# Optimization experiments

Measured on AMD Instinct MI355X. Metric: run time of the kernel, lower is better.

## Reference

```python
import jax, jax.numpy as jnp
import numpy as np

N, E, C, EC, L = 50000, 600000, 128, 16, 4
LN_EPS = 1e-5


def setup_inputs() -> dict:
    key = jax.random.key(0)
    ks = jax.random.split(key, 10)
    return {
        "x": jax.random.normal(ks[0], (N, C), jnp.float32),
        "edge_attr": jax.random.normal(ks[1], (E, EC), jnp.float32),
        "We": jax.random.normal(ks[2], (EC, C), jnp.float32) / np.sqrt(EC).astype(np.float32),
        "be": jnp.zeros((C,), jnp.float32),
        "W1": jax.random.normal(ks[3], (L, C, C), jnp.float32) / np.sqrt(C).astype(np.float32),
        "b1": jnp.zeros((L, C), jnp.float32),
        "W2": jax.random.normal(ks[4], (L, C, C), jnp.float32) / np.sqrt(C).astype(np.float32),
        "b2": jnp.zeros((L, C), jnp.float32),
        "gamma": jnp.ones((L, C), jnp.float32),
        "beta": jnp.zeros((L, C), jnp.float32),
        "edge_index": jax.random.randint(ks[5], (2, E), 0, N, dtype=jnp.int32),
    }


def reference(x, edge_attr, We, be, W1, b1, W2, b2, gamma, beta, edge_index):
    src = edge_index[0]  # x_j (message source)
    dst = edge_index[1]  # aggregation target
    # lin_edge: Linear + SiLU, shared across layers
    ea = jax.nn.silu(edge_attr @ We + be)  # [E, C]
    n = x.shape[0]
    for l in range(L):
        # GINEConv message: ReLU(x_j + edge_attr), scatter-sum to target nodes
        msg = jax.nn.relu(x[src] + ea)                       # [E, C]
        agg = jax.ops.segment_sum(msg, dst, num_segments=n)  # [N, C]
        h = x + agg  # (1 + eps) * x + agg, eps = 0
        # GINEConv nn: Linear -> SiLU -> Linear
        h = jax.nn.silu(h @ W1[l] + b1[l]) @ W2[l] + b2[l]
        # residual + LayerNorm
        y = x + h
        mu = y.mean(-1, keepdims=True)
        var = y.var(-1, keepdims=True)
        x = (y - mu) * jax.lax.rsqrt(var + LN_EPS) * gamma[l] + beta[l]
    return x
```

## Files before the change

kernel.cpp:

```cpp
#include <hip/hip_runtime.h>

#define NN 50000
#define EE 600000
#define CC 128
#define ECC 16
#define LL 4
#define LN_EPS 1e-5f
#define MTILE 80
#define PADC 136
#define YSTR 132

typedef float f32x4 __attribute__((ext_vector_type(4)));
typedef short bf16x8 __attribute__((ext_vector_type(8)));

static __device__ __forceinline__ float bf2f(unsigned short u) {
  union { unsigned int i; float f; } v; v.i = ((unsigned int)u) << 16; return v.f;
}
static __device__ __forceinline__ unsigned short f2bf(float f) {
  union { float f; unsigned int i; } v; v.f = f;
  unsigned int b = v.i + 0x7FFFu + ((v.i >> 16) & 1u);
  return (unsigned short)(b >> 16);
}
static __device__ __forceinline__ float silu_f(float v) {
  return v / (1.f + __expf(-v));
}


__global__ void count_kernel(const int* __restrict__ dst, int* __restrict__ counts, int E) {
  int e = blockIdx.x * blockDim.x + threadIdx.x;
  if (e < E) atomicAdd(&counts[dst[e]], 1);
}

__global__ __launch_bounds__(1024) void scan1_kernel(const int* __restrict__ counts,
                                                     int* __restrict__ bsum, int n) {
  __shared__ int wsum[16];
  const int tid = threadIdx.x, lane = tid & 63, wv = tid >> 6;
  const int i = blockIdx.x * 1024 + tid;
  int s = (i < n) ? counts[i] : 0;
  #pragma unroll
  for (int off = 1; off < 64; off <<= 1) s += __shfl_xor(s, off);
  if (lane == 0) wsum[wv] = s;
  __syncthreads();
  if (tid == 0) {
    int t = 0;
    #pragma unroll
    for (int j = 0; j < 16; ++j) t += wsum[j];
    bsum[blockIdx.x] = t;
  }
}

__global__ void scan2_kernel(const int* __restrict__ bsum, int* __restrict__ boff, int nb) {
  const int lane = threadIdx.x;
  int v = (lane < nb) ? bsum[lane] : 0;
  int incl = v;
  #pragma unroll
  for (int off = 1; off < 64; off <<= 1) {
    int t = __shfl_up(incl, off);
    if (lane >= off) incl += t;
  }
  if (lane < nb) boff[lane] = incl - v;
}

__global__ __launch_bounds__(1024) void scan3_kernel(const int* __restrict__ counts,
                                                     const int* __restrict__ boff,
                                                     int* __restrict__ rowptr, int n) {
  __shared__ int wsum[16];
  const int tid = threadIdx.x, lane = tid & 63, wv = tid >> 6;
  const int i = blockIdx.x * 1024 + tid;
  const int v = (i < n) ? counts[i] : 0;
  int incl = v;
  #pragma unroll
  for (int off = 1; off < 64; off <<= 1) {
    int t = __shfl_up(incl, off);
    if (lane >= off) incl += t;
  }
  if (lane == 63) wsum[wv] = incl;
  __syncthreads();
  if (wv == 0) {
    int vv = (lane < 16) ? wsum[lane] : 0;
    int vi = vv;
    #pragma unroll
    for (int off = 1; off < 16; off <<= 1) {
      int t = __shfl_up(vi, off);
      if (lane >= off) vi += t;
    }
    if (lane < 16) wsum[lane] = vi - vv;
  }
  __syncthreads();
  if (i < n) rowptr[i + 1] = boff[blockIdx.x] + wsum[wv] + incl;
  if (i == 0) rowptr[0] = 0;
}

__global__ void fill_kernel(const int* __restrict__ src, const int* __restrict__ dst,
                            const int* __restrict__ rowptr, int* __restrict__ cursor,
                            int* __restrict__ eidx, int* __restrict__ esrc, int E) {
  int e = blockIdx.x * blockDim.x + threadIdx.x;
  if (e < E) {
    const int d = dst[e];
    const int pos = rowptr[d] + atomicAdd(&cursor[d], 1);
    eidx[pos] = e;
    esrc[pos] = src[e];
  }
}


__global__ void webconv_kernel(const float* __restrict__ We, unsigned short* __restrict__ webf) {
  const int t = blockIdx.x * blockDim.x + threadIdx.x;
  if (t >= 8 * 64 * 8) return;
  const int j = t & 7, l = (t >> 3) & 63, cg = t >> 9;
  const int k = (l >> 4) * 8 + j, c = cg * 16 + (l & 15);
  webf[t] = (k < 16) ? f2bf(We[k * CC + c]) : (unsigned short)0;
}


__global__ __launch_bounds__(256) void ea_kernel(const float* __restrict__ edge_attr,
                                                 const unsigned short* __restrict__ webf,
                                                 const float* __restrict__ be,
                                                 const int* __restrict__ eidx,
                                                 unsigned short* __restrict__ ea) {
  __shared__ float er[64][20];
  __shared__ unsigned short eaT[64 * 132];
  const int tid = threadIdx.x;
  const int lane = tid & 63, wv = tid >> 6;

  bf16x8 bw[8];
  #pragma unroll
  for (int cg = 0; cg < 8; ++cg)
    bw[cg] = *(const bf16x8*)(webf + cg * 512 + lane * 8);
  float bev[8];
  #pragma unroll
  for (int cg = 0; cg < 8; ++cg) bev[cg] = be[cg * 16 + (lane & 15)];

  const int base = blockIdx.x * 64;
  {
    const int r = tid >> 2, q = tid & 3;
    const int e = eidx[base + r];
    *(float4*)(&er[r][q * 4]) = *(const float4*)(edge_attr + (size_t)e * ECC + q * 4);
  }
  __syncthreads();

  const int arow = wv * 16 + (lane & 15);
  const int ko = lane >> 4;
  union { unsigned short u[8]; bf16x8 v; } afu;
  if (ko < 2) {
    #pragma unroll
    for (int j = 0; j < 8; ++j) afu.u[j] = f2bf(er[arow][ko * 8 + j]);
  } else {
    #pragma unroll
    for (int j = 0; j < 8; ++j) afu.u[j] = 0;
  }

  f32x4 acc[8];
  #pragma unroll
  for (int cg = 0; cg < 8; ++cg) {
    acc[cg] = (f32x4)0.f;
    acc[cg] = __builtin_amdgcn_mfma_f32_16x16x32_bf16(afu.v, bw[cg], acc[cg], 0, 0, 0);
  }

  const int rl0 = wv * 16 + ko * 4;
  const int cb = lane & 15;
  #pragma unroll
  for (int cg = 0; cg < 8; ++cg)
    #pragma unroll
    for (int r = 0; r < 4; ++r) {
      const float v = acc[cg][r] + bev[cg];
      eaT[(rl0 + r) * 132 + cg * 16 + cb] = f2bf(silu_f(v));
    }
  __syncthreads();

  uint4* eg = (uint4*)(ea + (size_t)base * CC);
  #pragma unroll
  for (int k = 0; k < 4; ++k) {
    const int u = tid + k * 256;
    const int row = u >> 4, ch = u & 15;
    eg[u] = *(const uint4*)(&eaT[row * 132 + ch * 8]);
  }
}


__global__ __launch_bounds__(128) void wconv_kernel(const float* __restrict__ W1,
                                                    const float* __restrict__ W2,
                                                    unsigned short* __restrict__ wt) {
  const int b = blockIdx.x;
  const int c = b & (CC - 1);
  const int mat = (b >> 7) & 1;
  const int l = b >> 8;
  const float* W = (mat ? W2 : W1) + (size_t)l * CC * CC;
  unsigned short* o = wt + ((size_t)l * 2 + mat) * CC * CC + (size_t)c * CC;
  const int k = threadIdx.x;
  o[k] = f2bf(W[(size_t)k * CC + c]);
}


__global__ __launch_bounds__(256) void agg4_kernel(const float* __restrict__ x_in,
                                                   unsigned short* __restrict__ h_out,
                                                   const unsigned short* __restrict__ ea,
                                                   const int* __restrict__ rowptr,
                                                   const int* __restrict__ esrc) {
  const int tid = threadIdx.x;
  const int lane = tid & 63;
  const int half = lane >> 5;
  const int l32 = lane & 31;
  const int c0 = l32 * 4;
  const int wv = tid >> 6;
  const int n = blockIdx.x * 4 + wv;

  const int p0 = rowptr[n], p1 = rowptr[n + 1];
  float a0 = 0.f, a1 = 0.f, a2 = 0.f, a3 = 0.f;

  int p = p0 + half;
  for (; p + 2 < p1; p += 4) {
    const int s0 = esrc[p], s1 = esrc[p + 2];
    const float4 x0 = *(const float4*)(x_in + (size_t)s0 * CC + c0);
    const float4 x1 = *(const float4*)(x_in + (size_t)s1 * CC + c0);
    const uint2 e0 = *(const uint2*)(ea + (size_t)p * CC + c0);
    const uint2 e1 = *(const uint2*)(ea + (size_t)(p + 2) * CC + c0);
    a0 += fmaxf(x0.x + bf2f((unsigned short)e0.x), 0.f)
        + fmaxf(x1.x + bf2f((unsigned short)e1.x), 0.f);
    a1 += fmaxf(x0.y + bf2f((unsigned short)(e0.x >> 16)), 0.f)
        + fmaxf(x1.y + bf2f((unsigned short)(e1.x >> 16)), 0.f);
    a2 += fmaxf(x0.z + bf2f((unsigned short)e0.y), 0.f)
        + fmaxf(x1.z + bf2f((unsigned short)e1.y), 0.f);
    a3 += fmaxf(x0.w + bf2f((unsigned short)(e0.y >> 16)), 0.f)
        + fmaxf(x1.w + bf2f((unsigned short)(e1.y >> 16)), 0.f);
  }
  if (p < p1) {
    const int s0 = esrc[p];
    const float4 x0 = *(const float4*)(x_in + (size_t)s0 * CC + c0);
    const uint2 e0 = *(const uint2*)(ea + (size_t)p * CC + c0);
    a0 += fmaxf(x0.x + bf2f((unsigned short)e0.x), 0.f);
    a1 += fmaxf(x0.y + bf2f((unsigned short)(e0.x >> 16)), 0.f);
    a2 += fmaxf(x0.z + bf2f((unsigned short)e0.y), 0.f);
    a3 += fmaxf(x0.w + bf2f((unsigned short)(e0.y >> 16)), 0.f);
  }

  a0 += __shfl_xor(a0, 32);
  a1 += __shfl_xor(a1, 32);
  a2 += __shfl_xor(a2, 32);
  a3 += __shfl_xor(a3, 32);

  if (half == 0) {
    const float4 xs = *(const float4*)(x_in + (size_t)n * CC + c0);
    uint2 pk;
    pk.x = (unsigned int)f2bf(xs.x + a0) | ((unsigned int)f2bf(xs.y + a1) << 16);
    pk.y = (unsigned int)f2bf(xs.z + a2) | ((unsigned int)f2bf(xs.w + a3) << 16);
    *(uint2*)(h_out + (size_t)n * CC + c0) = pk;
  }
}


__global__ __launch_bounds__(256) void agg_fb_kernel(const float* __restrict__ x_in,
                                                     unsigned short* __restrict__ h_out,
                                                     const float* __restrict__ edge_attr,
                                                     const float* __restrict__ We,
                                                     const float* __restrict__ be,
                                                     const int* __restrict__ rowptr,
                                                     const int* __restrict__ eidx,
                                                     const int* __restrict__ esrc) {
  const int tid = threadIdx.x;
  const int c = tid & (CC - 1);
  const int g = tid >> 7;
  const int n = blockIdx.x * 2 + g;

  float wec[ECC];
  #pragma unroll
  for (int k = 0; k < ECC; ++k) wec[k] = We[k * CC + c];
  const float bev = be[c];

  const int p0 = rowptr[n], p1 = rowptr[n + 1];
  float acc = 0.f;
  for (int p = p0; p < p1; ++p) {
    const int e0 = eidx[p];
    const int s0 = esrc[p];
    const float4* ar0 = (const float4*)(edge_attr + (size_t)e0 * ECC);
    const float4 a0 = ar0[0], a1 = ar0[1], a2 = ar0[2], a3 = ar0[3];
    float v0 = bev
      + a0.x*wec[0]  + a0.y*wec[1]  + a0.z*wec[2]  + a0.w*wec[3]
      + a1.x*wec[4]  + a1.y*wec[5]  + a1.z*wec[6]  + a1.w*wec[7]
      + a2.x*wec[8]  + a2.y*wec[9]  + a2.z*wec[10] + a2.w*wec[11]
      + a3.x*wec[12] + a3.y*wec[13] + a3.z*wec[14] + a3.w*wec[15];
    acc += fmaxf(x_in[(size_t)s0 * CC + c] + silu_f(v0), 0.f);
  }
  h_out[(size_t)n * CC + c] = f2bf(x_in[(size_t)n * CC + c] + acc);
}


__global__ __launch_bounds__(256) void mlp_kernel(const float* __restrict__ x_in,
                                                  const unsigned short* __restrict__ hbuf,
                                                  const unsigned short* __restrict__ wt1,
                                                  const unsigned short* __restrict__ wt2,
                                                  const float* __restrict__ b1,
                                                  const float* __restrict__ b2,
                                                  const float* __restrict__ gamma,
                                                  const float* __restrict__ beta,
                                                  float* __restrict__ x_out) {
  __shared__ __align__(16) char smem[MTILE * PADC * 2 * 2];
  unsigned short* hA = (unsigned short*)smem;
  unsigned short* tA = (unsigned short*)(smem + MTILE * PADC * 2);
  float* yS = (float*)smem;
  __shared__ float red[MTILE][4][2];

  const int tid = threadIdx.x;
  const int lane = tid & 63;
  const int wv = tid >> 6;
  const int node0 = blockIdx.x * MTILE;
  const int colq = lane & 15;
  const int krow = lane >> 4;
  const int colb = wv * 32;

  for (int idx = tid; idx < MTILE * 16; idx += 256) {
    const int row = idx >> 4, ch = idx & 15;
    *(uint4*)(&hA[row * PADC + ch * 8]) =
        *(const uint4*)(hbuf + (size_t)(node0 + row) * CC + ch * 8);
  }
  __syncthreads();

  bf16x8 bw[2][4];
  #pragma unroll
  for (int n2 = 0; n2 < 2; ++n2)
    #pragma unroll
    for (int kk = 0; kk < 4; ++kk)
      bw[n2][kk] = *(const bf16x8*)(wt1 + (size_t)(colb + n2 * 16 + colq) * CC + kk * 32 + krow * 8);

  f32x4 acc[5][2];
  #pragma unroll
  for (int m = 0; m < 5; ++m) { acc[m][0] = (f32x4)0.f; acc[m][1] = (f32x4)0.f; }

  #pragma unroll
  for (int m = 0; m < 5; ++m)
    #pragma unroll
    for (int kk = 0; kk < 4; ++kk) {
      const bf16x8 a = *(const bf16x8*)(&hA[(m * 16 + colq) * PADC + kk * 32 + krow * 8]);
      acc[m][0] = __builtin_amdgcn_mfma_f32_16x16x32_bf16(a, bw[0][kk], acc[m][0], 0, 0, 0);
      acc[m][1] = __builtin_amdgcn_mfma_f32_16x16x32_bf16(a, bw[1][kk], acc[m][1], 0, 0, 0);
    }

  const float b1v0 = b1[colb + colq], b1v1 = b1[colb + 16 + colq];
  #pragma unroll
  for (int m = 0; m < 5; ++m)
    #pragma unroll
    for (int r = 0; r < 4; ++r) {
      const int row = m * 16 + krow * 4 + r;
      tA[row * PADC + colb + colq]      = f2bf(silu_f(acc[m][0][r] + b1v0));
      tA[row * PADC + colb + 16 + colq] = f2bf(silu_f(acc[m][1][r] + b1v1));
    }
  __syncthreads();

  #pragma unroll
  for (int n2 = 0; n2 < 2; ++n2)
    #pragma unroll
    for (int kk = 0; kk < 4; ++kk)
      bw[n2][kk] = *(const bf16x8*)(wt2 + (size_t)(colb + n2 * 16 + colq) * CC + kk * 32 + krow * 8);

  f32x4 acc2[5][2];
  #pragma unroll
  for (int m = 0; m < 5; ++m) { acc2[m][0] = (f32x4)0.f; acc2[m][1] = (f32x4)0.f; }

  #pragma unroll
  for (int m = 0; m < 5; ++m)
    #pragma unroll
    for (int kk = 0; kk < 4; ++kk) {
      const bf16x8 a = *(const bf16x8*)(&tA[(m * 16 + colq) * PADC + kk * 32 + krow * 8]);
      acc2[m][0] = __builtin_amdgcn_mfma_f32_16x16x32_bf16(a, bw[0][kk], acc2[m][0], 0, 0, 0);
      acc2[m][1] = __builtin_amdgcn_mfma_f32_16x16x32_bf16(a, bw[1][kk], acc2[m][1], 0, 0, 0);
    }

  const float b2v0 = b2[colb + colq], b2v1 = b2[colb + 16 + colq];
  float yv[5][2][4];
  #pragma unroll
  for (int m = 0; m < 5; ++m)
    #pragma unroll
    for (int r = 0; r < 4; ++r) {
      const int row = m * 16 + krow * 4 + r;
      yv[m][0][r] = acc2[m][0][r] + b2v0 + x_in[(size_t)(node0 + row) * CC + colb + colq];
      yv[m][1][r] = acc2[m][1][r] + b2v1 + x_in[(size_t)(node0 + row) * CC + colb + 16 + colq];
    }

  #pragma unroll
  for (int m = 0; m < 5; ++m)
    #pragma unroll
    for (int r = 0; r < 4; ++r) {
      float s = yv[m][0][r] + yv[m][1][r];
      float s2 = yv[m][0][r] * yv[m][0][r] + yv[m][1][r] * yv[m][1][r];
      #pragma unroll
      for (int off = 1; off < 16; off <<= 1) {
        s  += __shfl_xor(s, off);
        s2 += __shfl_xor(s2, off);
      }
      if (colq == 0) {
        const int row = m * 16 + krow * 4 + r;
        red[row][wv][0] = s;
        red[row][wv][1] = s2;
      }
    }
  __syncthreads();

  const float gm0 = gamma[colb + colq], gm1 = gamma[colb + 16 + colq];
  const float bt0 = beta[colb + colq],  bt1 = beta[colb + 16 + colq];
  #pragma unroll
  for (int m = 0; m < 5; ++m)
    #pragma unroll
    for (int r = 0; r < 4; ++r) {
      const int row = m * 16 + krow * 4 + r;
      const float s  = red[row][0][0] + red[row][1][0] + red[row][2][0] + red[row][3][0];
      const float s2 = red[row][0][1] + red[row][1][1] + red[row][2][1] + red[row][3][1];
      const float mean = s * (1.f / 128.f);
      const float var = s2 * (1.f / 128.f) - mean * mean;
      const float rstd = rsqrtf(var + LN_EPS);
      yS[row * YSTR + colb + colq]      = (yv[m][0][r] - mean) * rstd * gm0 + bt0;
      yS[row * YSTR + colb + 16 + colq] = (yv[m][1][r] - mean) * rstd * gm1 + bt1;
    }
  __syncthreads();

  float* og = x_out + (size_t)node0 * CC;
  #pragma unroll
  for (int k = 0; k < 10; ++k) {
    const int u = tid + k * 256;
    const int row = u >> 5, q = u & 31;
    *(float4*)(og + u * 4) = *(const float4*)(&yS[row * YSTR + q * 4]);
  }
}


extern "C" void kernel_launch(void* const* d_in, const int* in_sizes, int n_in,
                              void* d_out, int out_size, void* d_ws, size_t ws_size,
                              hipStream_t stream) {
  const float* x         = (const float*)d_in[0];
  const float* edge_attr = (const float*)d_in[1];
  const float* We        = (const float*)d_in[2];
  const float* be        = (const float*)d_in[3];
  const float* W1        = (const float*)d_in[4];
  const float* b1        = (const float*)d_in[5];
  const float* W2        = (const float*)d_in[6];
  const float* b2        = (const float*)d_in[7];
  const float* gamma     = (const float*)d_in[8];
  const float* beta      = (const float*)d_in[9];
  const int*   ei        = (const int*)d_in[10];
  const int*   src       = ei;
  const int*   dst       = ei + EE;
  float* out = (float*)d_out;

  char* ws = (char*)d_ws;
  float*          xbuf   = (float*)(ws + 0);
  unsigned short* hbuf   = (unsigned short*)(ws + 25600000);
  unsigned short* wt     = (unsigned short*)(ws + 38400000);
  int*            counts = (int*)(ws + 38662400);
  int*            rowptr = (int*)(ws + 38862592);
  int*            cursor = (int*)(ws + 39062784);
  int*            eidx   = (int*)(ws + 39262976);
  int*            esrc   = (int*)(ws + 41663232);
  unsigned short* ea     = (unsigned short*)(ws + 44063232);
  unsigned short* webf   = (unsigned short*)(ws + 39062784);
  int*            bsum   = (int*)(ws + 39262976);
  int*            boff   = (int*)(ws + 39262976 + 256);
  const bool use_ea = (ws_size >= 197663232ull);
  const int NB = (NN + 1023) / 1024;

  hipMemsetAsync(counts, 0, (size_t)NN * 4, stream);
  hipMemsetAsync(cursor, 0, (size_t)NN * 4, stream);
  count_kernel<<<(EE + 255) / 256, 256, 0, stream>>>(dst, counts, EE);
  scan1_kernel<<<NB, 1024, 0, stream>>>(counts, bsum, NN);
  scan2_kernel<<<1, 64, 0, stream>>>(bsum, boff, NB);
  scan3_kernel<<<NB, 1024, 0, stream>>>(counts, boff, rowptr, NN);
  fill_kernel<<<(EE + 255) / 256, 256, 0, stream>>>(src, dst, rowptr, cursor, eidx, esrc, EE);
  wconv_kernel<<<LL * 2 * CC, 128, 0, stream>>>(W1, W2, wt);
  if (use_ea) {
    webconv_kernel<<<16, 256, 0, stream>>>(We, webf);
    ea_kernel<<<EE / 64, 256, 0, stream>>>(edge_attr, webf, be, eidx, ea);
  }

  const float* xin = x;
  float* bufs[LL] = { xbuf, out, xbuf, out };
  for (int l = 0; l < LL; ++l) {
    float* xo = bufs[l];
    if (use_ea)
      agg4_kernel<<<NN / 4, 256, 0, stream>>>(xin, hbuf, ea, rowptr, esrc);
    else
      agg_fb_kernel<<<NN / 2, 256, 0, stream>>>(xin, hbuf, edge_attr, We, be, rowptr, eidx, esrc);
    mlp_kernel<<<NN / MTILE, 256, 0, stream>>>(
        xin, hbuf,
        wt + ((size_t)l * 2) * CC * CC, wt + ((size_t)l * 2 + 1) * CC * CC,
        b1 + (size_t)l * CC, b2 + (size_t)l * CC,
        gamma + (size_t)l * CC, beta + (size_t)l * CC, xo);
    xin = xo;
  }
}
```

Baseline: 491.5 us.

## Recompute edge embeddings per layer inside aggregation instead of materializing them

```diff
diff --git a/kernel.cpp b/kernel.cpp
--- a/kernel.cpp
+++ b/kernel.cpp
@@ -9,6 +9,7 @@
 #define MTILE 80
 #define PADC 136
 #define YSTR 132
+#define ESTR 132
 
 typedef float f32x4 __attribute__((ext_vector_type(4)));
 typedef short bf16x8 __attribute__((ext_vector_type(8)));
@@ -104,77 +105,24 @@
 }
 
 
+__global__ __launch_bounds__(256) void gather_attr_kernel(const float* __restrict__ edge_attr,
+                                                          const int* __restrict__ eidx,
+                                                          float* __restrict__ attr_csr) {
+  const long t = (long)blockIdx.x * 256 + threadIdx.x;
+  if (t >= (long)EE * 4) return;
+  const int p = (int)(t >> 2), q = (int)(t & 3);
+  const int e = eidx[p];
+  *(float4*)(attr_csr + (size_t)p * ECC + q * 4) =
+      *(const float4*)(edge_attr + (size_t)e * ECC + q * 4);
+}
+
+
 __global__ void webconv_kernel(const float* __restrict__ We, unsigned short* __restrict__ webf) {
   const int t = blockIdx.x * blockDim.x + threadIdx.x;
   if (t >= 8 * 64 * 8) return;
   const int j = t & 7, l = (t >> 3) & 63, cg = t >> 9;
   const int k = (l >> 4) * 8 + j, c = cg * 16 + (l & 15);
   webf[t] = (k < 16) ? f2bf(We[k * CC + c]) : (unsigned short)0;
-}
-
-
-__global__ __launch_bounds__(256) void ea_kernel(const float* __restrict__ edge_attr,
-                                                 const unsigned short* __restrict__ webf,
-                                                 const float* __restrict__ be,
-                                                 const int* __restrict__ eidx,
-                                                 unsigned short* __restrict__ ea) {
-  __shared__ float er[64][20];
-  __shared__ unsigned short eaT[64 * 132];
-  const int tid = threadIdx.x;
-  const int lane = tid & 63, wv = tid >> 6;
-
-  bf16x8 bw[8];
-  #pragma unroll
-  for (int cg = 0; cg < 8; ++cg)
-    bw[cg] = *(const bf16x8*)(webf + cg * 512 + lane * 8);
-  float bev[8];
-  #pragma unroll
-  for (int cg = 0; cg < 8; ++cg) bev[cg] = be[cg * 16 + (lane & 15)];
-
-  const int base = blockIdx.x * 64;
-  {
-    const int r = tid >> 2, q = tid & 3;
-    const int e = eidx[base + r];
-    *(float4*)(&er[r][q * 4]) = *(const float4*)(edge_attr + (size_t)e * ECC + q * 4);
-  }
-  __syncthreads();
-
-  const int arow = wv * 16 + (lane & 15);
-  const int ko = lane >> 4;
-  union { unsigned short u[8]; bf16x8 v; } afu;
-  if (ko < 2) {
-    #pragma unroll
-    for (int j = 0; j < 8; ++j) afu.u[j] = f2bf(er[arow][ko * 8 + j]);
-  } else {
-    #pragma unroll
-    for (int j = 0; j < 8; ++j) afu.u[j] = 0;
-  }
-
-  f32x4 acc[8];
-  #pragma unroll
-  for (int cg = 0; cg < 8; ++cg) {
-    acc[cg] = (f32x4)0.f;
-    acc[cg] = __builtin_amdgcn_mfma_f32_16x16x32_bf16(afu.v, bw[cg], acc[cg], 0, 0, 0);
-  }
-
-  const int rl0 = wv * 16 + ko * 4;
-  const int cb = lane & 15;
-  #pragma unroll
-  for (int cg = 0; cg < 8; ++cg)
-    #pragma unroll
-    for (int r = 0; r < 4; ++r) {
-      const float v = acc[cg][r] + bev[cg];
-      eaT[(rl0 + r) * 132 + cg * 16 + cb] = f2bf(silu_f(v));
-    }
-  __syncthreads();
-
-  uint4* eg = (uint4*)(ea + (size_t)base * CC);
-  #pragma unroll
-  for (int k = 0; k < 4; ++k) {
-    const int u = tid + k * 256;
-    const int row = u >> 4, ch = u & 15;
-    eg[u] = *(const uint4*)(&eaT[row * 132 + ch * 8]);
-  }
 }
 
 
@@ -192,46 +140,79 @@
 }
 
 
-__global__ __launch_bounds__(256) void agg4_kernel(const float* __restrict__ x_in,
+__global__ __launch_bounds__(256) void agg5_kernel(const float* __restrict__ x_in,
                                                    unsigned short* __restrict__ h_out,
-                                                   const unsigned short* __restrict__ ea,
+                                                   const float* __restrict__ attr_csr,
+                                                   const unsigned short* __restrict__ webf,
+                                                   const float* __restrict__ be,
                                                    const int* __restrict__ rowptr,
                                                    const int* __restrict__ esrc) {
+  __shared__ unsigned short ealds[4][16 * ESTR];
   const int tid = threadIdx.x;
   const int lane = tid & 63;
-  const int half = lane >> 5;
-  const int l32 = lane & 31;
+  const int wv = tid >> 6;
+  const int l16 = lane & 15, ko = lane >> 4;
+  const int half = lane >> 5, l32 = lane & 31;
   const int c0 = l32 * 4;
-  const int wv = tid >> 6;
+  unsigned short* elds = ealds[wv];
+
+  bf16x8 bw[8];
+  #pragma unroll
+  for (int cg = 0; cg < 8; ++cg)
+    bw[cg] = *(const bf16x8*)(webf + cg * 512 + lane * 8);
+  float bev[8];
+  #pragma unroll
+  for (int cg = 0; cg < 8; ++cg) bev[cg] = be[cg * 16 + l16];
+
   const int n = blockIdx.x * 4 + wv;
-
   const int p0 = rowptr[n], p1 = rowptr[n + 1];
   float a0 = 0.f, a1 = 0.f, a2 = 0.f, a3 = 0.f;
 
-  int p = p0 + half;
-  for (; p + 2 < p1; p += 4) {
-    const int s0 = esrc[p], s1 = esrc[p + 2];
-    const float4 x0 = *(const float4*)(x_in + (size_t)s0 * CC + c0);
-    const float4 x1 = *(const float4*)(x_in + (size_t)s1 * CC + c0);
-    const uint2 e0 = *(const uint2*)(ea + (size_t)p * CC + c0);
-    const uint2 e1 = *(const uint2*)(ea + (size_t)(p + 2) * CC + c0);
-    a0 += fmaxf(x0.x + bf2f((unsigned short)e0.x), 0.f)
-        + fmaxf(x1.x + bf2f((unsigned short)e1.x), 0.f);
-    a1 += fmaxf(x0.y + bf2f((unsigned short)(e0.x >> 16)), 0.f)
-        + fmaxf(x1.y + bf2f((unsigned short)(e1.x >> 16)), 0.f);
-    a2 += fmaxf(x0.z + bf2f((unsigned short)e0.y), 0.f)
-        + fmaxf(x1.z + bf2f((unsigned short)e1.y), 0.f);
-    a3 += fmaxf(x0.w + bf2f((unsigned short)(e0.y >> 16)), 0.f)
-        + fmaxf(x1.w + bf2f((unsigned short)(e1.y >> 16)), 0.f);
-  }
-  if (p < p1) {
-    const int s0 = esrc[p];
-    const float4 x0 = *(const float4*)(x_in + (size_t)s0 * CC + c0);
-    const uint2 e0 = *(const uint2*)(ea + (size_t)p * CC + c0);
-    a0 += fmaxf(x0.x + bf2f((unsigned short)e0.x), 0.f);
-    a1 += fmaxf(x0.y + bf2f((unsigned short)(e0.x >> 16)), 0.f);
-    a2 += fmaxf(x0.z + bf2f((unsigned short)e0.y), 0.f);
-    a3 += fmaxf(x0.w + bf2f((unsigned short)(e0.y >> 16)), 0.f);
+  for (int pb = p0; pb < p1; pb += 16) {
+    const int nb = (p1 - pb < 16) ? (p1 - pb) : 16;
+
+    union { unsigned short u[8]; bf16x8 v; } af;
+    if (ko < 2 && l16 < nb) {
+      const float* ap = attr_csr + (size_t)(pb + l16) * ECC + ko * 8;
+      const float4 q0 = *(const float4*)ap;
+      const float4 q1 = *(const float4*)(ap + 4);
+      af.u[0] = f2bf(q0.x); af.u[1] = f2bf(q0.y);
+      af.u[2] = f2bf(q0.z); af.u[3] = f2bf(q0.w);
+      af.u[4] = f2bf(q1.x); af.u[5] = f2bf(q1.y);
+      af.u[6] = f2bf(q1.z); af.u[7] = f2bf(q1.w);
+    } else {
+      #pragma unroll
+      for (int j = 0; j < 8; ++j) af.u[j] = 0;
+    }
+
+    f32x4 acc[8];
+    #pragma unroll
+    for (int cg = 0; cg < 8; ++cg) {
+      acc[cg] = (f32x4)0.f;
+      acc[cg] = __builtin_amdgcn_mfma_f32_16x16x32_bf16(af.v, bw[cg], acc[cg], 0, 0, 0);
+    }
+
+    asm volatile("s_waitcnt lgkmcnt(0)" ::: "memory");
+
+    #pragma unroll
+    for (int cg = 0; cg < 8; ++cg)
+      #pragma unroll
+      for (int r = 0; r < 4; ++r) {
+        const float v = acc[cg][r] + bev[cg];
+        elds[(ko * 4 + r) * ESTR + cg * 16 + l16] = f2bf(silu_f(v));
+      }
+    asm volatile("s_waitcnt lgkmcnt(0)" ::: "memory");
+
+    for (int e = half; e < nb; e += 2) {
+      const int p = pb + e;
+      const int s = esrc[p];
+      const float4 xv = *(const float4*)(x_in + (size_t)s * CC + c0);
+      const uint2 ev = *(const uint2*)(elds + e * ESTR + c0);
+      a0 += fmaxf(xv.x + bf2f((unsigned short)ev.x), 0.f);
+      a1 += fmaxf(xv.y + bf2f((unsigned short)(ev.x >> 16)), 0.f);
+      a2 += fmaxf(xv.z + bf2f((unsigned short)ev.y), 0.f);
+      a3 += fmaxf(xv.w + bf2f((unsigned short)(ev.y >> 16)), 0.f);
+    }
   }
 
   a0 += __shfl_xor(a0, 32);
@@ -449,11 +430,11 @@
   int*            cursor = (int*)(ws + 39062784);
   int*            eidx   = (int*)(ws + 39262976);
   int*            esrc   = (int*)(ws + 41663232);
-  unsigned short* ea     = (unsigned short*)(ws + 44063232);
+  float*          attr_csr = (float*)(ws + 44063232);
   unsigned short* webf   = (unsigned short*)(ws + 39062784);
   int*            bsum   = (int*)(ws + 39262976);
   int*            boff   = (int*)(ws + 39262976 + 256);
-  const bool use_ea = (ws_size >= 197663232ull);
+  const bool use_fast = (ws_size >= 82463232ull);
   const int NB = (NN + 1023) / 1024;
 
   hipMemsetAsync(counts, 0, (size_t)NN * 4, stream);
@@ -464,17 +445,17 @@
   scan3_kernel<<<NB, 1024, 0, stream>>>(counts, boff, rowptr, NN);
   fill_kernel<<<(EE + 255) / 256, 256, 0, stream>>>(src, dst, rowptr, cursor, eidx, esrc, EE);
   wconv_kernel<<<LL * 2 * CC, 128, 0, stream>>>(W1, W2, wt);
-  if (use_ea) {
+  if (use_fast) {
     webconv_kernel<<<16, 256, 0, stream>>>(We, webf);
-    ea_kernel<<<EE / 64, 256, 0, stream>>>(edge_attr, webf, be, eidx, ea);
+    gather_attr_kernel<<<(EE * 4 + 255) / 256, 256, 0, stream>>>(edge_attr, eidx, attr_csr);
   }
 
   const float* xin = x;
   float* bufs[LL] = { xbuf, out, xbuf, out };
   for (int l = 0; l < LL; ++l) {
     float* xo = bufs[l];
-    if (use_ea)
-      agg4_kernel<<<NN / 4, 256, 0, stream>>>(xin, hbuf, ea, rowptr, esrc);
+    if (use_fast)
+      agg5_kernel<<<NN / 4, 256, 0, stream>>>(xin, hbuf, attr_csr, webf, be, rowptr, esrc);
     else
       agg_fb_kernel<<<NN / 2, 256, 0, stream>>>(xin, hbuf, edge_attr, We, be, rowptr, eidx, esrc);
     mlp_kernel<<<NN / MTILE, 256, 0, stream>>>(
```

After: 662.3 us. 34.7% more time.

## Store node features in bf16 to halve gather traffic in aggregation

Applied to the files above, without the earlier changes.

```diff
diff --git a/kernel.cpp b/kernel.cpp
--- a/kernel.cpp
+++ b/kernel.cpp
@@ -101,6 +101,21 @@
     eidx[pos] = e;
     esrc[pos] = src[e];
   }
+}
+
+
+__global__ __launch_bounds__(256) void xconv_kernel(const float* __restrict__ x,
+                                                    unsigned short* __restrict__ xb) {
+  const int t = blockIdx.x * 256 + threadIdx.x;
+  if (t >= NN * CC / 8) return;
+  const float4 a = ((const float4*)x)[t * 2];
+  const float4 b = ((const float4*)x)[t * 2 + 1];
+  uint4 o;
+  o.x = (unsigned)f2bf(a.x) | ((unsigned)f2bf(a.y) << 16);
+  o.y = (unsigned)f2bf(a.z) | ((unsigned)f2bf(a.w) << 16);
+  o.z = (unsigned)f2bf(b.x) | ((unsigned)f2bf(b.y) << 16);
+  o.w = (unsigned)f2bf(b.z) | ((unsigned)f2bf(b.w) << 16);
+  ((uint4*)xb)[t] = o;
 }
 
 
@@ -192,7 +207,7 @@
 }
 
 
-__global__ __launch_bounds__(256) void agg4_kernel(const float* __restrict__ x_in,
+__global__ __launch_bounds__(256) void agg4_kernel(const unsigned short* __restrict__ xb,
                                                    unsigned short* __restrict__ h_out,
                                                    const unsigned short* __restrict__ ea,
                                                    const int* __restrict__ rowptr,
@@ -209,29 +224,41 @@
   float a0 = 0.f, a1 = 0.f, a2 = 0.f, a3 = 0.f;
 
   int p = p0 + half;
-  for (; p + 2 < p1; p += 4) {
-    const int s0 = esrc[p], s1 = esrc[p + 2];
-    const float4 x0 = *(const float4*)(x_in + (size_t)s0 * CC + c0);
-    const float4 x1 = *(const float4*)(x_in + (size_t)s1 * CC + c0);
+  for (; p + 6 < p1; p += 8) {
+    const int s0 = esrc[p], s1 = esrc[p + 2], s2 = esrc[p + 4], s3 = esrc[p + 6];
+    const uint2 x0 = *(const uint2*)(xb + (size_t)s0 * CC + c0);
+    const uint2 x1 = *(const uint2*)(xb + (size_t)s1 * CC + c0);
+    const uint2 x2 = *(const uint2*)(xb + (size_t)s2 * CC + c0);
+    const uint2 x3 = *(const uint2*)(xb + (size_t)s3 * CC + c0);
     const uint2 e0 = *(const uint2*)(ea + (size_t)p * CC + c0);
     const uint2 e1 = *(const uint2*)(ea + (size_t)(p + 2) * CC + c0);
-    a0 += fmaxf(x0.x + bf2f((unsigned short)e0.x), 0.f)
-        + fmaxf(x1.x + bf2f((unsigned short)e1.x), 0.f);
-    a1 += fmaxf(x0.y + bf2f((unsigned short)(e0.x >> 16)), 0.f)
-        + fmaxf(x1.y + bf2f((unsigned short)(e1.x >> 16)), 0.f);
-    a2 += fmaxf(x0.z + bf2f((unsigned short)e0.y), 0.f)
-        + fmaxf(x1.z + bf2f((unsigned short)e1.y), 0.f);
-    a3 += fmaxf(x0.w + bf2f((unsigned short)(e0.y >> 16)), 0.f)
-        + fmaxf(x1.w + bf2f((unsigned short)(e1.y >> 16)), 0.f);
-  }
-  if (p < p1) {
+    const uint2 e2 = *(const uint2*)(ea + (size_t)(p + 4) * CC + c0);
+    const uint2 e3 = *(const uint2*)(ea + (size_t)(p + 6) * CC + c0);
+    a0 += fmaxf(bf2f((unsigned short)x0.x) + bf2f((unsigned short)e0.x), 0.f)
+        + fmaxf(bf2f((unsigned short)x1.x) + bf2f((unsigned short)e1.x), 0.f)
+        + fmaxf(bf2f((unsigned short)x2.x) + bf2f((unsigned short)e2.x), 0.f)
+        + fmaxf(bf2f((unsigned short)x3.x) + bf2f((unsigned short)e3.x), 0.f);
+    a1 += fmaxf(bf2f((unsigned short)(x0.x >> 16)) + bf2f((unsigned short)(e0.x >> 16)), 0.f)
+        + fmaxf(bf2f((unsigned short)(x1.x >> 16)) + bf2f((unsigned short)(e1.x >> 16)), 0.f)
+        + fmaxf(bf2f((unsigned short)(x2.x >> 16)) + bf2f((unsigned short)(e2.x >> 16)), 0.f)
+        + fmaxf(bf2f((unsigned short)(x3.x >> 16)) + bf2f((unsigned short)(e3.x >> 16)), 0.f);
+    a2 += fmaxf(bf2f((unsigned short)x0.y) + bf2f((unsigned short)e0.y), 0.f)
+        + fmaxf(bf2f((unsigned short)x1.y) + bf2f((unsigned short)e1.y), 0.f)
+        + fmaxf(bf2f((unsigned short)x2.y) + bf2f((unsigned short)e2.y), 0.f)
+        + fmaxf(bf2f((unsigned short)x3.y) + bf2f((unsigned short)e3.y), 0.f);
+    a3 += fmaxf(bf2f((unsigned short)(x0.y >> 16)) + bf2f((unsigned short)(e0.y >> 16)), 0.f)
+        + fmaxf(bf2f((unsigned short)(x1.y >> 16)) + bf2f((unsigned short)(e1.y >> 16)), 0.f)
+        + fmaxf(bf2f((unsigned short)(x2.y >> 16)) + bf2f((unsigned short)(e2.y >> 16)), 0.f)
+        + fmaxf(bf2f((unsigned short)(x3.y >> 16)) + bf2f((unsigned short)(e3.y >> 16)), 0.f);
+  }
+  for (; p < p1; p += 2) {
     const int s0 = esrc[p];
-    const float4 x0 = *(const float4*)(x_in + (size_t)s0 * CC + c0);
+    const uint2 x0 = *(const uint2*)(xb + (size_t)s0 * CC + c0);
     const uint2 e0 = *(const uint2*)(ea + (size_t)p * CC + c0);
-    a0 += fmaxf(x0.x + bf2f((unsigned short)e0.x), 0.f);
-    a1 += fmaxf(x0.y + bf2f((unsigned short)(e0.x >> 16)), 0.f);
-    a2 += fmaxf(x0.z + bf2f((unsigned short)e0.y), 0.f);
-    a3 += fmaxf(x0.w + bf2f((unsigned short)(e0.y >> 16)), 0.f);
+    a0 += fmaxf(bf2f((unsigned short)x0.x) + bf2f((unsigned short)e0.x), 0.f);
+    a1 += fmaxf(bf2f((unsigned short)(x0.x >> 16)) + bf2f((unsigned short)(e0.x >> 16)), 0.f);
+    a2 += fmaxf(bf2f((unsigned short)x0.y) + bf2f((unsigned short)e0.y), 0.f);
+    a3 += fmaxf(bf2f((unsigned short)(x0.y >> 16)) + bf2f((unsigned short)(e0.y >> 16)), 0.f);
   }
 
   a0 += __shfl_xor(a0, 32);
@@ -240,16 +267,18 @@
   a3 += __shfl_xor(a3, 32);
 
   if (half == 0) {
-    const float4 xs = *(const float4*)(x_in + (size_t)n * CC + c0);
+    const uint2 xs = *(const uint2*)(xb + (size_t)n * CC + c0);
     uint2 pk;
-    pk.x = (unsigned int)f2bf(xs.x + a0) | ((unsigned int)f2bf(xs.y + a1) << 16);
-    pk.y = (unsigned int)f2bf(xs.z + a2) | ((unsigned int)f2bf(xs.w + a3) << 16);
+    pk.x = (unsigned)f2bf(bf2f((unsigned short)xs.x) + a0)
+         | ((unsigned)f2bf(bf2f((unsigned short)(xs.x >> 16)) + a1) << 16);
+    pk.y = (unsigned)f2bf(bf2f((unsigned short)xs.y) + a2)
+         | ((unsigned)f2bf(bf2f((unsigned short)(xs.y >> 16)) + a3) << 16);
     *(uint2*)(h_out + (size_t)n * CC + c0) = pk;
   }
 }
 
 
-__global__ __launch_bounds__(256) void agg_fb_kernel(const float* __restrict__ x_in,
+__global__ __launch_bounds__(256) void agg_fb_kernel(const unsigned short* __restrict__ xb,
                                                      unsigned short* __restrict__ h_out,
                                                      const float* __restrict__ edge_attr,
                                                      const float* __restrict__ We,
@@ -279,13 +308,14 @@
       + a1.x*wec[4]  + a1.y*wec[5]  + a1.z*wec[6]  + a1.w*wec[7]
       + a2.x*wec[8]  + a2.y*wec[9]  + a2.z*wec[10] + a2.w*wec[11]
       + a3.x*wec[12] + a3.y*wec[13] + a3.z*wec[14] + a3.w*wec[15];
-    acc += fmaxf(x_in[(size_t)s0 * CC + c] + silu_f(v0), 0.f);
-  }
-  h_out[(size_t)n * CC + c] = f2bf(x_in[(size_t)n * CC + c] + acc);
-}
-
-
-__global__ __launch_bounds__(256) void mlp_kernel(const float* __restrict__ x_in,
+    acc += fmaxf(bf2f(xb[(size_t)s0 * CC + c]) + silu_f(v0), 0.f);
+  }
+  h_out[(size_t)n * CC + c] = f2bf(bf2f(xb[(size_t)n * CC + c]) + acc);
+}
+
+
+template <int FINAL>
+__global__ __launch_bounds__(256) void mlp_kernel(unsigned short* xb,
                                                   const unsigned short* __restrict__ hbuf,
                                                   const unsigned short* __restrict__ wt1,
                                                   const unsigned short* __restrict__ wt2,
@@ -293,7 +323,7 @@
                                                   const float* __restrict__ b2,
                                                   const float* __restrict__ gamma,
                                                   const float* __restrict__ beta,
-                                                  float* __restrict__ x_out) {
+                                                  float* __restrict__ out) {
   __shared__ __align__(16) char smem[MTILE * PADC * 2 * 2];
   unsigned short* hA = (unsigned short*)smem;
   unsigned short* tA = (unsigned short*)(smem + MTILE * PADC * 2);
@@ -372,8 +402,8 @@
     #pragma unroll
     for (int r = 0; r < 4; ++r) {
       const int row = m * 16 + krow * 4 + r;
-      yv[m][0][r] = acc2[m][0][r] + b2v0 + x_in[(size_t)(node0 + row) * CC + colb + colq];
-      yv[m][1][r] = acc2[m][1][r] + b2v1 + x_in[(size_t)(node0 + row) * CC + colb + 16 + colq];
+      yv[m][0][r] = acc2[m][0][r] + b2v0 + bf2f(xb[(size_t)(node0 + row) * CC + colb + colq]);
+      yv[m][1][r] = acc2[m][1][r] + b2v1 + bf2f(xb[(size_t)(node0 + row) * CC + colb + 16 + colq]);
     }
 
   #pragma unroll
@@ -412,12 +442,28 @@
     }
   __syncthreads();
 
-  float* og = x_out + (size_t)node0 * CC;
-  #pragma unroll
-  for (int k = 0; k < 10; ++k) {
-    const int u = tid + k * 256;
-    const int row = u >> 5, q = u & 31;
-    *(float4*)(og + u * 4) = *(const float4*)(&yS[row * YSTR + q * 4]);
+  if (FINAL) {
+    float* og = out + (size_t)node0 * CC;
+    #pragma unroll
+    for (int k = 0; k < 10; ++k) {
+      const int u = tid + k * 256;
+      const int row = u >> 5, q = u & 31;
+      *(float4*)(og + u * 4) = *(const float4*)(&yS[row * YSTR + q * 4]);
+    }
+  } else {
+    unsigned short* xg = xb + (size_t)node0 * CC;
+    #pragma unroll
+    for (int k = 0; k < 5; ++k) {
+      const int u = tid + k * 256;
+      const int row = u >> 4, ch8 = u & 15;
+      const float* yp = &yS[row * YSTR + ch8 * 8];
+      uint4 o;
+      o.x = (unsigned)f2bf(yp[0]) | ((unsigned)f2bf(yp[1]) << 16);
+      o.y = (unsigned)f2bf(yp[2]) | ((unsigned)f2bf(yp[3]) << 16);
+      o.z = (unsigned)f2bf(yp[4]) | ((unsigned)f2bf(yp[5]) << 16);
+      o.w = (unsigned)f2bf(yp[6]) | ((unsigned)f2bf(yp[7]) << 16);
+      *(uint4*)(xg + u * 8) = o;
+    }
   }
 }
 
@@ -441,19 +487,19 @@
   float* out = (float*)d_out;
 
   char* ws = (char*)d_ws;
-  float*          xbuf   = (float*)(ws + 0);
-  unsigned short* hbuf   = (unsigned short*)(ws + 25600000);
-  unsigned short* wt     = (unsigned short*)(ws + 38400000);
-  int*            counts = (int*)(ws + 38662400);
-  int*            rowptr = (int*)(ws + 38862592);
-  int*            cursor = (int*)(ws + 39062784);
-  int*            eidx   = (int*)(ws + 39262976);
-  int*            esrc   = (int*)(ws + 41663232);
-  unsigned short* ea     = (unsigned short*)(ws + 44063232);
-  unsigned short* webf   = (unsigned short*)(ws + 39062784);
-  int*            bsum   = (int*)(ws + 39262976);
-  int*            boff   = (int*)(ws + 39262976 + 256);
-  const bool use_ea = (ws_size >= 197663232ull);
+  unsigned short* xbf    = (unsigned short*)(ws + 0);
+  unsigned short* hbuf   = (unsigned short*)(ws + 12800000);
+  unsigned short* wt     = (unsigned short*)(ws + 25600000);
+  int*            counts = (int*)(ws + 25862400);
+  int*            rowptr = (int*)(ws + 26062592);
+  int*            cursor = (int*)(ws + 26262784);
+  int*            eidx   = (int*)(ws + 26462976);
+  int*            esrc   = (int*)(ws + 28863232);
+  unsigned short* ea     = (unsigned short*)(ws + 31263360);
+  unsigned short* webf   = (unsigned short*)(ws + 26262784);
+  int*            bsum   = (int*)(ws + 26462976);
+  int*            boff   = (int*)(ws + 26462976 + 256);
+  const bool use_ea = (ws_size >= 184863360ull);
   const int NB = (NN + 1023) / 1024;
 
   hipMemsetAsync(counts, 0, (size_t)NN * 4, stream);
@@ -464,24 +510,26 @@
   scan3_kernel<<<NB, 1024, 0, stream>>>(counts, boff, rowptr, NN);
   fill_kernel<<<(EE + 255) / 256, 256, 0, stream>>>(src, dst, rowptr, cursor, eidx, esrc, EE);
   wconv_kernel<<<LL * 2 * CC, 128, 0, stream>>>(W1, W2, wt);
+  xconv_kernel<<<(NN * CC / 8 + 255) / 256, 256, 0, stream>>>(x, xbf);
   if (use_ea) {
     webconv_kernel<<<16, 256, 0, stream>>>(We, webf);
     ea_kernel<<<EE / 64, 256, 0, stream>>>(edge_attr, webf, be, eidx, ea);
   }
 
-  const float* xin = x;
-  float* bufs[LL] = { xbuf, out, xbuf, out };
   for (int l = 0; l < LL; ++l) {
-    float* xo = bufs[l];
     if (use_ea)
-      agg4_kernel<<<NN / 4, 256, 0, stream>>>(xin, hbuf, ea, rowptr, esrc);
+      agg4_kernel<<<NN / 4, 256, 0, stream>>>(xbf, hbuf, ea, rowptr, esrc);
     else
-      agg_fb_kernel<<<NN / 2, 256, 0, stream>>>(xin, hbuf, edge_attr, We, be, rowptr, eidx, esrc);
-    mlp_kernel<<<NN / MTILE, 256, 0, stream>>>(
-        xin, hbuf,
-        wt + ((size_t)l * 2) * CC * CC, wt + ((size_t)l * 2 + 1) * CC * CC,
-        b1 + (size_t)l * CC, b2 + (size_t)l * CC,
-        gamma + (size_t)l * CC, beta + (size_t)l * CC, xo);
-    xin = xo;
-  }
-}
+      agg_fb_kernel<<<NN / 2, 256, 0, stream>>>(xbf, hbuf, edge_attr, We, be, rowptr, eidx, esrc);
+    const unsigned short* w1p = wt + ((size_t)l * 2) * CC * CC;
+    const unsigned short* w2p = wt + ((size_t)l * 2 + 1) * CC * CC;
+    const float* b1p = b1 + (size_t)l * CC;
+    const float* b2p = b2 + (size_t)l * CC;
+    const float* gmp = gamma + (size_t)l * CC;
+    const float* btp = beta + (size_t)l * CC;
+    if (l == LL - 1)
+      mlp_kernel<1><<<NN / MTILE, 256, 0, stream>>>(xbf, hbuf, w1p, w2p, b1p, b2p, gmp, btp, out);
+    else
+      mlp_kernel<0><<<NN / MTILE, 256, 0, stream>>>(xbf, hbuf, w1p, w2p, b1p, b2p, gmp, btp, out);
+  }
+}
```

New measurement: 415.9 us. 15.4% less time.
